# Kernel tuning notes

Measured on AMD Instinct MI355X. Metric: run time of the kernel, lower is better.

Reference implementation:

```python
import jax, jax.numpy as jnp
import numpy as np

N_NODES = 100000
D_FEAT = 128
N_EDGES = 1600000
N_ROWS = 50000  # batch of target nodes


def setup_inputs() -> dict:
    key = jax.random.key(0)
    k1, k2, k3 = jax.random.split(key, 3)
    features = jax.random.normal(k1, (N_NODES, D_FEAT), dtype=jnp.float32)
    neigh_ids = jax.random.randint(k2, (N_EDGES,), 0, N_NODES, dtype=jnp.int64)
    row_ids = jnp.sort(jax.random.randint(k3, (N_EDGES,), 0, N_ROWS, dtype=jnp.int64))
    return {
        "features": features,
        "neigh_ids": neigh_ids,
        "row_ids": row_ids,
        "num_segments": N_ROWS,
    }


def reference(features, neigh_ids, row_ids, num_segments):
    # Gather neighbor embeddings: [E, D]
    gathered = features[neigh_ids]
    # Per-row sum and count -> mean (matches mask.mm with values 1/deg)
    sums = jax.ops.segment_sum(gathered, row_ids, num_segments=num_segments)
    counts = jax.ops.segment_sum(
        jnp.ones((neigh_ids.shape[0],), dtype=features.dtype),
        row_ids,
        num_segments=num_segments,
    )
    to_feats = sums / jnp.maximum(counts, 1.0)[:, None]
    return to_feats
```

## Files before the change

### kernel.cpp

```cpp
#include <hip/hip_runtime.h>

#define D_FEAT 128
#define WAVE 64

__device__ __forceinline__ unsigned short f32_to_bf16_rn(float f) {
    unsigned int u = __float_as_uint(f);
    unsigned int r = u + 0x7fffu + ((u >> 16) & 1u);
    return (unsigned short)(r >> 16);
}

__global__ void prep_kernel(const float* __restrict__ feats,
                            unsigned short* __restrict__ tbl,
                            int n_elems, int total,
                            const int* __restrict__ rids,
                            int* __restrict__ row_start,
                            int n_edges, int n_rows, int grid_c) {
    if ((int)blockIdx.x < grid_c) {
        int i = (blockIdx.x * blockDim.x + threadIdx.x) * 8;
        if (i >= total) return;
        if (i + 8 <= n_elems) {
            float4 a = *(const float4*)(feats + i);
            float4 b = *(const float4*)(feats + i + 4);
            uint4 o;
            o.x = (unsigned)f32_to_bf16_rn(a.x) | ((unsigned)f32_to_bf16_rn(a.y) << 16);
            o.y = (unsigned)f32_to_bf16_rn(a.z) | ((unsigned)f32_to_bf16_rn(a.w) << 16);
            o.z = (unsigned)f32_to_bf16_rn(b.x) | ((unsigned)f32_to_bf16_rn(b.y) << 16);
            o.w = (unsigned)f32_to_bf16_rn(b.z) | ((unsigned)f32_to_bf16_rn(b.w) << 16);
            *(uint4*)(tbl + i) = o;
        } else {
            for (int k = 0; k < 8 && i + k < total; ++k)
                tbl[i + k] = (i + k < n_elems) ? f32_to_bf16_rn(feats[i + k])
                                               : (unsigned short)0;
        }
    } else {
        int e = (blockIdx.x - grid_c) * blockDim.x + threadIdx.x;
        if (e >= n_edges) return;
        int r_cur  = rids[e];
        int r_prev = (e == 0) ? -1 : rids[e - 1];
        for (int r = r_prev + 1; r <= r_cur; ++r) row_start[r] = e;
        if (e == n_edges - 1) {
            for (int r = r_cur + 1; r <= n_rows; ++r) row_start[r] = n_edges;
        }
    }
}

__global__ void __launch_bounds__(256)
mean_agg_kernel(const uint4* __restrict__ tbl4,
                const int* __restrict__ nids,
                const int* __restrict__ row_start,
                float* __restrict__ out,
                int n_rows, int zero_row) {
    int wave = (blockIdx.x * blockDim.x + threadIdx.x) >> 6;
    int lane = threadIdx.x & (WAVE - 1);
    if (wave >= n_rows) return;

    const int q   = lane >> 4;
    const int sub = lane & 15;

    int lo = row_start[wave];
    int hi = row_start[wave + 1];

    float acc[8];
    #pragma unroll
    for (int k = 0; k < 8; ++k) acc[k] = 0.f;

    int e = lo;
    for (; e + 32 <= hi; e += 32) {
        int myid = nids[e + (lane & 31)];
        uint4 u[8];
        #pragma unroll
        for (int g = 0; g < 8; ++g) {
            int nid = __shfl(myid, 4 * g + q, WAVE);
            u[g] = tbl4[((unsigned)nid << 4) + (unsigned)sub];
        }
        #pragma unroll
        for (int g = 0; g < 8; ++g) {
            acc[0] += __uint_as_float(u[g].x << 16);
            acc[1] += __uint_as_float(u[g].x & 0xffff0000u);
            acc[2] += __uint_as_float(u[g].y << 16);
            acc[3] += __uint_as_float(u[g].y & 0xffff0000u);
            acc[4] += __uint_as_float(u[g].z << 16);
            acc[5] += __uint_as_float(u[g].z & 0xffff0000u);
            acc[6] += __uint_as_float(u[g].w << 16);
            acc[7] += __uint_as_float(u[g].w & 0xffff0000u);
        }
    }
    #pragma unroll
    for (int half_blk = 0; half_blk < 2; ++half_blk) {
        if (e < hi) {
            #pragma unroll
            for (int g = 0; g < 4; ++g) {
                int idx = e + 4 * g + q;
                int idc = idx < hi ? idx : hi - 1;
                int nid = nids[idc];
                nid = idx < hi ? nid : zero_row;
                uint4 u = tbl4[((unsigned)nid << 4) + (unsigned)sub];
                acc[0] += __uint_as_float(u.x << 16);
                acc[1] += __uint_as_float(u.x & 0xffff0000u);
                acc[2] += __uint_as_float(u.y << 16);
                acc[3] += __uint_as_float(u.y & 0xffff0000u);
                acc[4] += __uint_as_float(u.z << 16);
                acc[5] += __uint_as_float(u.z & 0xffff0000u);
                acc[6] += __uint_as_float(u.w << 16);
                acc[7] += __uint_as_float(u.w & 0xffff0000u);
            }
            e += 16;
        }
    }

    #pragma unroll
    for (int k = 0; k < 8; ++k) {
        acc[k] += __shfl_xor(acc[k], 16, WAVE);
        acc[k] += __shfl_xor(acc[k], 32, WAVE);
    }

    int deg = hi - lo;
    float inv = 1.0f / (float)(deg > 0 ? deg : 1);

    if (q < 2) {
        float4 o;
        o.x = (q == 0 ? acc[0] : acc[4]) * inv;
        o.y = (q == 0 ? acc[1] : acc[5]) * inv;
        o.z = (q == 0 ? acc[2] : acc[6]) * inv;
        o.w = (q == 0 ? acc[3] : acc[7]) * inv;
        *(float4*)(out + (size_t)wave * D_FEAT + sub * 8 + q * 4) = o;
    }
}

extern "C" void kernel_launch(void* const* d_in, const int* in_sizes, int n_in,
                              void* d_out, int out_size, void* d_ws, size_t ws_size,
                              hipStream_t stream) {
    const float* feats = (const float*)d_in[0];
    const int* nids    = (const int*)d_in[1];
    const int* rids    = (const int*)d_in[2];
    float* out         = (float*)d_out;

    int n_feat_elems = in_sizes[0];
    int n_nodes      = n_feat_elems / D_FEAT;
    int n_edges      = in_sizes[1];
    int n_rows       = out_size / D_FEAT;

    unsigned short* tbl = (unsigned short*)d_ws;
    size_t tbl_bytes = (size_t)(n_nodes + 1) * D_FEAT * sizeof(unsigned short);
    tbl_bytes = (tbl_bytes + 255) & ~(size_t)255;
    int* row_start = (int*)((char*)d_ws + tbl_bytes);

    const int BLOCK = 256;

    int total_tbl = (n_nodes + 1) * D_FEAT;
    int grid_c = ((total_tbl + 7) / 8 + BLOCK - 1) / BLOCK;
    int grid_b = (n_edges + BLOCK - 1) / BLOCK;
    prep_kernel<<<grid_c + grid_b, BLOCK, 0, stream>>>(feats, tbl, n_feat_elems,
                                                       total_tbl, rids, row_start,
                                                       n_edges, n_rows, grid_c);

    int waves_per_block = BLOCK / WAVE;
    int grid_a = (n_rows + waves_per_block - 1) / waves_per_block;
    mean_agg_kernel<<<grid_a, BLOCK, 0, stream>>>((const uint4*)tbl, nids, row_start,
                                                  out, n_rows, n_nodes);
}
```

Before: 154.6 us.

## Split bf16 feature table into column halves and run two passes per row

Stores the bf16 table as two separate 64-column halves, and launches two waves per output row, each gathering only its half. Each half-table is about 12.8 MB, so a pass's working set is more likely to stay in the cache hierarchy. Index loads and output stores now use nontemporal hints. The cost is twice as many waves and index reads, an extra shuffle reduction, and a shuffle-based output remap.

```diff
diff --git a/kernel.cpp b/kernel.cpp
--- a/kernel.cpp
+++ b/kernel.cpp
@@ -2,6 +2,8 @@
 
 #define D_FEAT 128
 #define WAVE 64
+
+typedef float f32x4 __attribute__((ext_vector_type(4)));
 
 __device__ __forceinline__ unsigned short f32_to_bf16_rn(float f) {
     unsigned int u = __float_as_uint(f);
@@ -9,29 +11,41 @@
     return (unsigned short)(r >> 16);
 }
 
+__device__ __forceinline__ void acc8(float (&acc)[8], uint4 u) {
+    acc[0] += __uint_as_float(u.x << 16);
+    acc[1] += __uint_as_float(u.x & 0xffff0000u);
+    acc[2] += __uint_as_float(u.y << 16);
+    acc[3] += __uint_as_float(u.y & 0xffff0000u);
+    acc[4] += __uint_as_float(u.z << 16);
+    acc[5] += __uint_as_float(u.z & 0xffff0000u);
+    acc[6] += __uint_as_float(u.w << 16);
+    acc[7] += __uint_as_float(u.w & 0xffff0000u);
+}
+
 __global__ void prep_kernel(const float* __restrict__ feats,
                             unsigned short* __restrict__ tbl,
-                            int n_elems, int total,
+                            int n_elems, int total, int half_elems,
                             const int* __restrict__ rids,
                             int* __restrict__ row_start,
                             int n_edges, int n_rows, int grid_c) {
     if ((int)blockIdx.x < grid_c) {
         int i = (blockIdx.x * blockDim.x + threadIdx.x) * 8;
         if (i >= total) return;
-        if (i + 8 <= n_elems) {
+        int node = i >> 7;
+        int c    = i & 127;
+        int dst  = (c >> 6) * half_elems + (node << 6) + (c & 63);
+        uint4 o;
+        if (i < n_elems) {
             float4 a = *(const float4*)(feats + i);
             float4 b = *(const float4*)(feats + i + 4);
-            uint4 o;
             o.x = (unsigned)f32_to_bf16_rn(a.x) | ((unsigned)f32_to_bf16_rn(a.y) << 16);
             o.y = (unsigned)f32_to_bf16_rn(a.z) | ((unsigned)f32_to_bf16_rn(a.w) << 16);
             o.z = (unsigned)f32_to_bf16_rn(b.x) | ((unsigned)f32_to_bf16_rn(b.y) << 16);
             o.w = (unsigned)f32_to_bf16_rn(b.z) | ((unsigned)f32_to_bf16_rn(b.w) << 16);
-            *(uint4*)(tbl + i) = o;
         } else {
-            for (int k = 0; k < 8 && i + k < total; ++k)
-                tbl[i + k] = (i + k < n_elems) ? f32_to_bf16_rn(feats[i + k])
-                                               : (unsigned short)0;
+            o.x = o.y = o.z = o.w = 0u;
         }
+        *(uint4*)(tbl + dst) = o;
     } else {
         int e = (blockIdx.x - grid_c) * blockDim.x + threadIdx.x;
         if (e >= n_edges) return;
@@ -49,13 +63,17 @@
                 const int* __restrict__ nids,
                 const int* __restrict__ row_start,
                 float* __restrict__ out,
-                int n_rows, int zero_row) {
-    int wave = (blockIdx.x * blockDim.x + threadIdx.x) >> 6;
+                int n_rows, int zero_row, int half_u4) {
+    int gw   = (blockIdx.x * blockDim.x + threadIdx.x) >> 6;
     int lane = threadIdx.x & (WAVE - 1);
+    int pass = (gw >= n_rows) ? 1 : 0;
+    int wave = gw - pass * n_rows;
     if (wave >= n_rows) return;
 
-    const int q   = lane >> 4;
-    const int sub = lane & 15;
+    const int oct = lane >> 3;
+    const int sub = lane & 7;
+
+    const uint4* __restrict__ tb = tbl4 + (size_t)pass * (size_t)half_u4;
 
     int lo = row_start[wave];
     int hi = row_start[wave + 1];
@@ -66,50 +84,31 @@
 
     int e = lo;
     for (; e + 32 <= hi; e += 32) {
-        int myid = nids[e + (lane & 31)];
-        uint4 u[8];
+        int myid = __builtin_nontemporal_load(nids + e + (lane & 31));
+        uint4 u[4];
         #pragma unroll
-        for (int g = 0; g < 8; ++g) {
-            int nid = __shfl(myid, 4 * g + q, WAVE);
-            u[g] = tbl4[((unsigned)nid << 4) + (unsigned)sub];
+        for (int g = 0; g < 4; ++g) {
+            int nid = __shfl(myid, 8 * g + oct, WAVE);
+            u[g] = tb[((unsigned)nid << 3) + (unsigned)sub];
         }
         #pragma unroll
-        for (int g = 0; g < 8; ++g) {
-            acc[0] += __uint_as_float(u[g].x << 16);
-            acc[1] += __uint_as_float(u[g].x & 0xffff0000u);
-            acc[2] += __uint_as_float(u[g].y << 16);
-            acc[3] += __uint_as_float(u[g].y & 0xffff0000u);
-            acc[4] += __uint_as_float(u[g].z << 16);
-            acc[5] += __uint_as_float(u[g].z & 0xffff0000u);
-            acc[6] += __uint_as_float(u[g].w << 16);
-            acc[7] += __uint_as_float(u[g].w & 0xffff0000u);
-        }
+        for (int g = 0; g < 4; ++g) acc8(acc, u[g]);
     }
     #pragma unroll
-    for (int half_blk = 0; half_blk < 2; ++half_blk) {
-        if (e < hi) {
-            #pragma unroll
-            for (int g = 0; g < 4; ++g) {
-                int idx = e + 4 * g + q;
-                int idc = idx < hi ? idx : hi - 1;
-                int nid = nids[idc];
-                nid = idx < hi ? nid : zero_row;
-                uint4 u = tbl4[((unsigned)nid << 4) + (unsigned)sub];
-                acc[0] += __uint_as_float(u.x << 16);
-                acc[1] += __uint_as_float(u.x & 0xffff0000u);
-                acc[2] += __uint_as_float(u.y << 16);
-                acc[3] += __uint_as_float(u.y & 0xffff0000u);
-                acc[4] += __uint_as_float(u.z << 16);
-                acc[5] += __uint_as_float(u.z & 0xffff0000u);
-                acc[6] += __uint_as_float(u.w << 16);
-                acc[7] += __uint_as_float(u.w & 0xffff0000u);
-            }
-            e += 16;
+    for (int g = 0; g < 4; ++g) {
+        if (e + 8 * g < hi) {
+            int idx = e + 8 * g + oct;
+            int idc = idx < hi ? idx : hi - 1;
+            int nid = nids[idc];
+            nid = idx < hi ? nid : zero_row;
+            uint4 u = tb[((unsigned)nid << 3) + (unsigned)sub];
+            acc8(acc, u);
         }
     }
 
     #pragma unroll
     for (int k = 0; k < 8; ++k) {
+        acc[k] += __shfl_xor(acc[k], 8, WAVE);
         acc[k] += __shfl_xor(acc[k], 16, WAVE);
         acc[k] += __shfl_xor(acc[k], 32, WAVE);
     }
@@ -117,13 +116,19 @@
     int deg = hi - lo;
     float inv = 1.0f / (float)(deg > 0 ? deg : 1);
 
-    if (q < 2) {
-        float4 o;
-        o.x = (q == 0 ? acc[0] : acc[4]) * inv;
-        o.y = (q == 0 ? acc[1] : acc[5]) * inv;
-        o.z = (q == 0 ? acc[2] : acc[6]) * inv;
-        o.w = (q == 0 ? acc[3] : acc[7]) * inv;
-        *(float4*)(out + (size_t)wave * D_FEAT + sub * 8 + q * 4) = o;
+    int srcl = (lane & 15) >> 1;
+    float o[4];
+    #pragma unroll
+    for (int k = 0; k < 4; ++k) {
+        float vlo = __shfl(acc[k],     srcl, WAVE);
+        float vhi = __shfl(acc[4 + k], srcl, WAVE);
+        o[k] = ((lane & 1) ? vhi : vlo) * inv;
+    }
+    if (lane < 16) {
+        f32x4 st;
+        st.x = o[0]; st.y = o[1]; st.z = o[2]; st.w = o[3];
+        __builtin_nontemporal_store(
+            st, (f32x4*)(out + (size_t)wave * D_FEAT + pass * 64 + lane * 4));
     }
 }
 
@@ -147,15 +152,20 @@
 
     const int BLOCK = 256;
 
+    int half_elems = (n_nodes + 1) * 64;
+    int half_u4    = (n_nodes + 1) * 8;
+
     int total_tbl = (n_nodes + 1) * D_FEAT;
     int grid_c = ((total_tbl + 7) / 8 + BLOCK - 1) / BLOCK;
     int grid_b = (n_edges + BLOCK - 1) / BLOCK;
     prep_kernel<<<grid_c + grid_b, BLOCK, 0, stream>>>(feats, tbl, n_feat_elems,
-                                                       total_tbl, rids, row_start,
+                                                       total_tbl, half_elems,
+                                                       rids, row_start,
                                                        n_edges, n_rows, grid_c);
 
     int waves_per_block = BLOCK / WAVE;
-    int grid_a = (n_rows + waves_per_block - 1) / waves_per_block;
+    int total_waves = 2 * n_rows;
+    int grid_a = (total_waves + waves_per_block - 1) / waves_per_block;
     mean_agg_kernel<<<grid_a, BLOCK, 0, stream>>>((const uint4*)tbl, nids, row_start,
-                                                  out, n_rows, n_nodes);
+                                                  out, n_rows, n_nodes, half_u4);
 }
```

After: 161.4 us. 1.04x slower.
